# Kernel optimization log

Hardware: AMD Instinct MI355X
Metric: run time of the kernel (lower is better)

## Reference

```python
import jax, jax.numpy as jnp
import numpy as np


def setup_inputs() -> dict:
    key = jax.random.key(0)
    k1, k2, k3, k4 = jax.random.split(key, 4)
    B, H, W, C, NCLS = 128, 14, 14, 512, 200
    # post-ReLU-like non-negative feature map
    x = jax.random.uniform(k1, (B, H, W, C), dtype=jnp.float32)
    # one-hot-like logits for ground-truth labels (only argmax is used)
    gt = jax.random.normal(k2, (B, NCLS), dtype=jnp.float32)
    # positional template codebook; index [H, W] (== shape[0]-1) is the sentinel
    # 'negative' template used for all-zero channels
    t_p = jax.random.normal(k3, (H + 1, W + 1, H, W), dtype=jnp.float32)
    # per-class channel template, broadcast-multiplied with masked features
    class_templates = jax.random.uniform(k4, (NCLS, H, W, C), dtype=jnp.float32)
    return {"x": x, "gt": gt, "t_p": t_p, "class_templates": class_templates}


def reference(x, gt, t_p, class_templates):
    # x: [B, H, W, C] channels-last feature map
    B, H, W, C = x.shape
    flat = x.reshape(B, H * W, C)
    # global spatial argmax per (batch, channel) == max_pool_with_argmax over full extent
    idx = jnp.argmax(flat, axis=1)            # [B, C]
    h = idx // W                               # [B, C]
    w = idx % W                                # [B, C]
    # channels whose spatial max is exactly 0 get the sentinel template index
    empty = jnp.max(flat, axis=1) == 0.0       # [B, C]
    sentinel = t_p.shape[0] - 1
    h = jnp.where(empty, sentinel, h)
    w = jnp.where(empty, sentinel, w)
    # gather positional templates: [B, C, H, W] -> [B, H, W, C]
    templates = jnp.transpose(t_p[h, w], (0, 2, 3, 1))
    masked = jax.nn.relu(x * templates)
    # training branch with gt, reduce_loss=False: mask by the class template
    cls = jnp.argmax(gt, axis=1)               # [B]
    masked = masked * class_templates[cls]     # [B, H, W, C]
    return (masked, x, templates)
```

## Files before the change

### kernel.cpp

```cpp
#include <hip/hip_runtime.h>

#define B    128
#define H    14
#define W    14
#define C    512
#define NCLS 200
#define HW   (H * W)
#define TP_DIM 15
#define SENT_OFF ((14 * TP_DIM + 14) * HW)

typedef float  v4f __attribute__((ext_vector_type(4)));
typedef int    v4i __attribute__((ext_vector_type(4)));

__global__ __launch_bounds__(512, 4) void fused_kernel(
        const float* __restrict__ x,
        const float* __restrict__ gt,
        const float* __restrict__ t_p,
        const float* __restrict__ ctpl,
        float*       __restrict__ out) {
    __shared__ v4f s_best[14][32];
    __shared__ v4i s_idx[14][32];
    __shared__ int s_off[128];
    __shared__ int s_cls;

    const int tid     = threadIdx.x;
    const int b       = blockIdx.x >> 2;
    const int quarter = blockIdx.x & 3;
    const int cg      = tid & 31;
    const int sl      = tid >> 5;
    const int c0      = quarter * 128 + cg * 4;

    const float* __restrict__ xp = x + (size_t)b * HW * C + c0;

    if (sl < 14) {
        const int sbeg = sl * 14;
        v4f best = *(const v4f*)(xp + (size_t)sbeg * C);
        v4i bidx = (v4i){sbeg, sbeg, sbeg, sbeg};
#pragma unroll
        for (int k = 1; k < 14; ++k) {
            const int s = sbeg + k;
            v4f v = *(const v4f*)(xp + (size_t)s * C);
            if (v.x > best.x) { best.x = v.x; bidx.x = s; }
            if (v.y > best.y) { best.y = v.y; bidx.y = s; }
            if (v.z > best.z) { best.z = v.z; bidx.z = s; }
            if (v.w > best.w) { best.w = v.w; bidx.w = s; }
        }
        s_best[sl][cg] = best;
        s_idx[sl][cg]  = bidx;
    } else {
        const int lane = tid - 448;
        const float* __restrict__ g = gt + (size_t)b * NCLS;
        float gb = -__builtin_inff();
        int   gi = NCLS;
        for (int i = lane; i < NCLS; i += 64) {
            float v = g[i];
            if (v > gb) { gb = v; gi = i; }
        }
#pragma unroll
        for (int d = 1; d < 64; d <<= 1) {
            float ov = __shfl_xor(gb, d);
            int   oi = __shfl_xor(gi, d);
            if (ov > gb || (ov == gb && oi < gi)) { gb = ov; gi = oi; }
        }
        if (lane == 0) s_cls = gi;
    }
    __syncthreads();

    if (tid < 32) {
        v4f cb = s_best[0][tid];
        v4i ci = s_idx[0][tid];
#pragma unroll
        for (int k = 1; k < 14; ++k) {
            v4f p = s_best[k][tid];
            v4i q = s_idx[k][tid];
            if (p.x > cb.x) { cb.x = p.x; ci.x = q.x; }
            if (p.y > cb.y) { cb.y = p.y; ci.y = q.y; }
            if (p.z > cb.z) { cb.z = p.z; ci.z = q.z; }
            if (p.w > cb.w) { cb.w = p.w; ci.w = q.w; }
        }
        v4i o;
        o.x = (cb.x == 0.0f) ? SENT_OFF : ((ci.x / W) * TP_DIM + (ci.x % W)) * HW;
        o.y = (cb.y == 0.0f) ? SENT_OFF : ((ci.y / W) * TP_DIM + (ci.y % W)) * HW;
        o.z = (cb.z == 0.0f) ? SENT_OFF : ((ci.z / W) * TP_DIM + (ci.z % W)) * HW;
        o.w = (cb.w == 0.0f) ? SENT_OFF : ((ci.w / W) * TP_DIM + (ci.w % W)) * HW;
        *(v4i*)&s_off[tid * 4] = o;
    }
    __syncthreads();

    const int klass = s_cls;
    const v4i off   = *(const v4i*)&s_off[cg * 4];

    const size_t plane = (size_t)B * HW * C;
    const float* __restrict__ ctp = ctpl + (size_t)klass * HW * C;

    for (int q = sl; q < 49; q += 16) {
        const int s0 = q * 4;

        v4f t0 = *(const v4f*)(t_p + off.x + s0);
        v4f t1 = *(const v4f*)(t_p + off.y + s0);
        v4f t2 = *(const v4f*)(t_p + off.z + s0);
        v4f t3 = *(const v4f*)(t_p + off.w + s0);
        v4f tv[4];
        tv[0] = (v4f){t0.x, t1.x, t2.x, t3.x};
        tv[1] = (v4f){t0.y, t1.y, t2.y, t3.y};
        tv[2] = (v4f){t0.z, t1.z, t2.z, t3.z};
        tv[3] = (v4f){t0.w, t1.w, t2.w, t3.w};

        const size_t base = ((size_t)b * HW + s0) * C + c0;
        const float* __restrict__ xq = x + base;
        const float* __restrict__ cp = ctp + (size_t)s0 * C + c0;
        float* __restrict__ out_m = out + base;
        float* __restrict__ out_x = out + plane + base;
        float* __restrict__ out_t = out + 2 * plane + base;

#pragma unroll
        for (int i = 0; i < 4; ++i) {
            v4f xv = *(const v4f*)(xq + (size_t)i * C);
            v4f ct = *(const v4f*)(cp + (size_t)i * C);
            v4f tt = tv[i];
            v4f m;
            m.x = fmaxf(xv.x * tt.x, 0.0f) * ct.x;
            m.y = fmaxf(xv.y * tt.y, 0.0f) * ct.y;
            m.z = fmaxf(xv.z * tt.z, 0.0f) * ct.z;
            m.w = fmaxf(xv.w * tt.w, 0.0f) * ct.w;
            __builtin_nontemporal_store(m,  (v4f*)(out_m + (size_t)i * C));
            __builtin_nontemporal_store(xv, (v4f*)(out_x + (size_t)i * C));
            __builtin_nontemporal_store(tt, (v4f*)(out_t + (size_t)i * C));
        }
    }
}

extern "C" void kernel_launch(void* const* d_in, const int* in_sizes, int n_in,
                              void* d_out, int out_size, void* d_ws, size_t ws_size,
                              hipStream_t stream) {
    const float* x    = (const float*)d_in[0];
    const float* gt   = (const float*)d_in[1];
    const float* t_p  = (const float*)d_in[2];
    const float* ctpl = (const float*)d_in[3];
    float* out = (float*)d_out;

    hipLaunchKernelGGL(fused_kernel,
                       dim3(4 * B), dim3(512), 0, stream,
                       x, gt, t_p, ctpl, out);
}
```

Baseline: 260.4 us.

## Stage gathered templates through LDS transpose and reorder block-to-batch mapping

Replaces the per-thread scattered 4-channel template gathers and register transpose with a cooperative load of each channel's template row into a shared-memory tile. The tile is aliased with the phase-1 reduction buffers through a union and filled in two halves. Later threads read it channel-contiguous. The block index mapping changes so consecutive blocks cover different batches of the same channel quarter, and the occupancy hint is removed from the launch bounds. This adds two extra barriers and LDS traffic, possibly with bank conflicts, in exchange for more coalesced global reads of t_p.

```diff
diff --git a/kernel.cpp b/kernel.cpp
--- a/kernel.cpp
+++ b/kernel.cpp
@@ -12,23 +12,26 @@
 typedef float  v4f __attribute__((ext_vector_type(4)));
 typedef int    v4i __attribute__((ext_vector_type(4)));
 
-__global__ __launch_bounds__(512, 4) void fused_kernel(
+__global__ __launch_bounds__(512) void fused_kernel(
         const float* __restrict__ x,
         const float* __restrict__ gt,
         const float* __restrict__ t_p,
         const float* __restrict__ ctpl,
         float*       __restrict__ out) {
-    __shared__ v4f s_best[14][32];
-    __shared__ v4i s_idx[14][32];
+    __shared__ union SMem {
+        struct { v4f best[14][32]; v4i idx[14][32]; } ph1;
+        float t_tile[100][128];
+    } smem;
     __shared__ int s_off[128];
     __shared__ int s_cls;
 
     const int tid     = threadIdx.x;
-    const int b       = blockIdx.x >> 2;
-    const int quarter = blockIdx.x & 3;
+    const int b       = blockIdx.x & 127;
+    const int quarter = blockIdx.x >> 7;
     const int cg      = tid & 31;
     const int sl      = tid >> 5;
     const int c0      = quarter * 128 + cg * 4;
+    const int cl      = cg * 4;
 
     const float* __restrict__ xp = x + (size_t)b * HW * C + c0;
 
@@ -45,8 +48,8 @@
             if (v.z > best.z) { best.z = v.z; bidx.z = s; }
             if (v.w > best.w) { best.w = v.w; bidx.w = s; }
         }
-        s_best[sl][cg] = best;
-        s_idx[sl][cg]  = bidx;
+        smem.ph1.best[sl][cg] = best;
+        smem.ph1.idx[sl][cg]  = bidx;
     } else {
         const int lane = tid - 448;
         const float* __restrict__ g = gt + (size_t)b * NCLS;
@@ -67,12 +70,12 @@
     __syncthreads();
 
     if (tid < 32) {
-        v4f cb = s_best[0][tid];
-        v4i ci = s_idx[0][tid];
+        v4f cb = smem.ph1.best[0][tid];
+        v4i ci = smem.ph1.idx[0][tid];
 #pragma unroll
         for (int k = 1; k < 14; ++k) {
-            v4f p = s_best[k][tid];
-            v4i q = s_idx[k][tid];
+            v4f p = smem.ph1.best[k][tid];
+            v4i q = smem.ph1.idx[k][tid];
             if (p.x > cb.x) { cb.x = p.x; ci.x = q.x; }
             if (p.y > cb.y) { cb.y = p.y; ci.y = q.y; }
             if (p.z > cb.z) { cb.z = p.z; ci.z = q.z; }
@@ -88,23 +91,30 @@
     __syncthreads();
 
     const int klass = s_cls;
-    const v4i off   = *(const v4i*)&s_off[cg * 4];
-
     const size_t plane = (size_t)B * HW * C;
     const float* __restrict__ ctp = ctpl + (size_t)klass * HW * C;
 
-    for (int q = sl; q < 49; q += 16) {
+    const int r = tid >> 2;
+    const int p = tid & 3;
+    const float* __restrict__ trow = t_p + s_off[r];
+
+    auto stage = [&](int jbeg, int jend, int sbase) {
+        for (int j = jbeg + p; j < jend; j += 4) {
+            v4f v = *(const v4f*)(trow + j * 4);
+            const int s = j * 4 - sbase;
+            smem.t_tile[s + 0][r] = v.x;
+            smem.t_tile[s + 1][r] = v.y;
+            smem.t_tile[s + 2][r] = v.z;
+            smem.t_tile[s + 3][r] = v.w;
+        }
+    };
+
+    auto process_quad = [&](int q, int sbase) {
         const int s0 = q * 4;
-
-        v4f t0 = *(const v4f*)(t_p + off.x + s0);
-        v4f t1 = *(const v4f*)(t_p + off.y + s0);
-        v4f t2 = *(const v4f*)(t_p + off.z + s0);
-        v4f t3 = *(const v4f*)(t_p + off.w + s0);
-        v4f tv[4];
-        tv[0] = (v4f){t0.x, t1.x, t2.x, t3.x};
-        tv[1] = (v4f){t0.y, t1.y, t2.y, t3.y};
-        tv[2] = (v4f){t0.z, t1.z, t2.z, t3.z};
-        tv[3] = (v4f){t0.w, t1.w, t2.w, t3.w};
+        v4f tvv[4];
+#pragma unroll
+        for (int i = 0; i < 4; ++i)
+            tvv[i] = *(const v4f*)&smem.t_tile[s0 - sbase + i][cl];
 
         const size_t base = ((size_t)b * HW + s0) * C + c0;
         const float* __restrict__ xq = x + base;
@@ -117,7 +127,7 @@
         for (int i = 0; i < 4; ++i) {
             v4f xv = *(const v4f*)(xq + (size_t)i * C);
             v4f ct = *(const v4f*)(cp + (size_t)i * C);
-            v4f tt = tv[i];
+            v4f tt = tvv[i];
             v4f m;
             m.x = fmaxf(xv.x * tt.x, 0.0f) * ct.x;
             m.y = fmaxf(xv.y * tt.y, 0.0f) * ct.y;
@@ -127,7 +137,18 @@
             __builtin_nontemporal_store(xv, (v4f*)(out_x + (size_t)i * C));
             __builtin_nontemporal_store(tt, (v4f*)(out_t + (size_t)i * C));
         }
-    }
+    };
+
+    stage(0, 24, 0);
+    __syncthreads();
+    process_quad(sl, 0);
+    if (sl < 8) process_quad(sl + 16, 0);
+    __syncthreads();
+
+    stage(24, 49, 96);
+    __syncthreads();
+    process_quad(24 + sl, 96);
+    if (sl <= 8) process_quad(40 + sl, 96);
 }
 
 extern "C" void kernel_launch(void* const* d_in, const int* in_sizes, int n_in,
```

Result: faster. 250.3 us (-3.9%).

## Keep x tile in registers across argmax and output phases, swizzle block order

Applied to the files above, without the earlier changes.

Each warp-row now loads its 12 (or 16) spatial rows of x into registers once, uses them for the per-thread argmax, and reuses them for the masked-output and x-copy writes instead of reading x again from global memory. All 16 warp-rows take part in the argmax, and the gt argmax moves to a separate wave after the first barrier. Block indexing changes so consecutive blocks cover different batches of the same channel quarter, and the occupancy hint in launch_bounds is dropped. The cost is many more live registers (the xr array), which may lower occupancy.

```diff
diff --git a/kernel.cpp b/kernel.cpp
--- a/kernel.cpp
+++ b/kernel.cpp
@@ -12,43 +12,85 @@
 typedef float  v4f __attribute__((ext_vector_type(4)));
 typedef int    v4i __attribute__((ext_vector_type(4)));
 
-__global__ __launch_bounds__(512, 4) void fused_kernel(
+__global__ __launch_bounds__(512) void fused_kernel(
         const float* __restrict__ x,
         const float* __restrict__ gt,
         const float* __restrict__ t_p,
         const float* __restrict__ ctpl,
         float*       __restrict__ out) {
-    __shared__ v4f s_best[14][32];
-    __shared__ v4i s_idx[14][32];
+    __shared__ v4f s_best[16][32];
+    __shared__ v4i s_idx[16][32];
     __shared__ int s_off[128];
     __shared__ int s_cls;
 
     const int tid     = threadIdx.x;
-    const int b       = blockIdx.x >> 2;
-    const int quarter = blockIdx.x & 3;
+    const int b       = blockIdx.x & 127;
+    const int quarter = blockIdx.x >> 7;
     const int cg      = tid & 31;
     const int sl      = tid >> 5;
     const int c0      = quarter * 128 + cg * 4;
+    const int cl      = cg * 4;
+    const bool extra  = (sl == 15);
+    const int  sbeg   = 12 * sl;
 
     const float* __restrict__ xp = x + (size_t)b * HW * C + c0;
 
-    if (sl < 14) {
-        const int sbeg = sl * 14;
-        v4f best = *(const v4f*)(xp + (size_t)sbeg * C);
-        v4i bidx = (v4i){sbeg, sbeg, sbeg, sbeg};
+    v4f xr[16];
 #pragma unroll
-        for (int k = 1; k < 14; ++k) {
+    for (int k = 0; k < 12; ++k)
+        xr[k] = *(const v4f*)(xp + (size_t)(sbeg + k) * C);
+    if (extra) {
+#pragma unroll
+        for (int k = 12; k < 16; ++k)
+            xr[k] = *(const v4f*)(xp + (size_t)(sbeg + k) * C);
+    }
+
+    v4f best = xr[0];
+    v4i bidx = (v4i){sbeg, sbeg, sbeg, sbeg};
+#pragma unroll
+    for (int k = 1; k < 12; ++k) {
+        const int s = sbeg + k;
+        v4f v = xr[k];
+        if (v.x > best.x) { best.x = v.x; bidx.x = s; }
+        if (v.y > best.y) { best.y = v.y; bidx.y = s; }
+        if (v.z > best.z) { best.z = v.z; bidx.z = s; }
+        if (v.w > best.w) { best.w = v.w; bidx.w = s; }
+    }
+    if (extra) {
+#pragma unroll
+        for (int k = 12; k < 16; ++k) {
             const int s = sbeg + k;
-            v4f v = *(const v4f*)(xp + (size_t)s * C);
+            v4f v = xr[k];
             if (v.x > best.x) { best.x = v.x; bidx.x = s; }
             if (v.y > best.y) { best.y = v.y; bidx.y = s; }
             if (v.z > best.z) { best.z = v.z; bidx.z = s; }
             if (v.w > best.w) { best.w = v.w; bidx.w = s; }
         }
-        s_best[sl][cg] = best;
-        s_idx[sl][cg]  = bidx;
-    } else {
-        const int lane = tid - 448;
+    }
+    s_best[sl][cg] = best;
+    s_idx[sl][cg]  = bidx;
+    __syncthreads();
+
+    if (tid < 32) {
+        v4f cb = s_best[0][tid];
+        v4i ci = s_idx[0][tid];
+#pragma unroll
+        for (int k = 1; k < 16; ++k) {
+            v4f p = s_best[k][tid];
+            v4i q = s_idx[k][tid];
+            if (p.x > cb.x) { cb.x = p.x; ci.x = q.x; }
+            if (p.y > cb.y) { cb.y = p.y; ci.y = q.y; }
+            if (p.z > cb.z) { cb.z = p.z; ci.z = q.z; }
+            if (p.w > cb.w) { cb.w = p.w; ci.w = q.w; }
+        }
+        v4i o;
+        o.x = (cb.x == 0.0f) ? SENT_OFF : ((ci.x / W) * TP_DIM + (ci.x % W)) * HW;
+        o.y = (cb.y == 0.0f) ? SENT_OFF : ((ci.y / W) * TP_DIM + (ci.y % W)) * HW;
+        o.z = (cb.z == 0.0f) ? SENT_OFF : ((ci.z / W) * TP_DIM + (ci.z % W)) * HW;
+        o.w = (cb.w == 0.0f) ? SENT_OFF : ((ci.w / W) * TP_DIM + (ci.w % W)) * HW;
+        *(v4i*)&s_off[tid * 4] = o;
+    } else if (tid >= 64 && tid < 128) {
+        const int lane = tid - 64;
         const float* __restrict__ g = gt + (size_t)b * NCLS;
         float gb = -__builtin_inff();
         int   gi = NCLS;
@@ -66,48 +108,32 @@
     }
     __syncthreads();
 
-    if (tid < 32) {
-        v4f cb = s_best[0][tid];
-        v4i ci = s_idx[0][tid];
+    const int klass = s_cls;
+    const v4i off = *(const v4i*)&s_off[cl];
+
+    v4f tr[4][4];
 #pragma unroll
-        for (int k = 1; k < 14; ++k) {
-            v4f p = s_best[k][tid];
-            v4i q = s_idx[k][tid];
-            if (p.x > cb.x) { cb.x = p.x; ci.x = q.x; }
-            if (p.y > cb.y) { cb.y = p.y; ci.y = q.y; }
-            if (p.z > cb.z) { cb.z = p.z; ci.z = q.z; }
-            if (p.w > cb.w) { cb.w = p.w; ci.w = q.w; }
-        }
-        v4i o;
-        o.x = (cb.x == 0.0f) ? SENT_OFF : ((ci.x / W) * TP_DIM + (ci.x % W)) * HW;
-        o.y = (cb.y == 0.0f) ? SENT_OFF : ((ci.y / W) * TP_DIM + (ci.y % W)) * HW;
-        o.z = (cb.z == 0.0f) ? SENT_OFF : ((ci.z / W) * TP_DIM + (ci.z % W)) * HW;
-        o.w = (cb.w == 0.0f) ? SENT_OFF : ((ci.w / W) * TP_DIM + (ci.w % W)) * HW;
-        *(v4i*)&s_off[tid * 4] = o;
+    for (int m = 0; m < 3; ++m) {
+        tr[0][m] = *(const v4f*)(t_p + off.x + sbeg + 4 * m);
+        tr[1][m] = *(const v4f*)(t_p + off.y + sbeg + 4 * m);
+        tr[2][m] = *(const v4f*)(t_p + off.z + sbeg + 4 * m);
+        tr[3][m] = *(const v4f*)(t_p + off.w + sbeg + 4 * m);
     }
-    __syncthreads();
-
-    const int klass = s_cls;
-    const v4i off   = *(const v4i*)&s_off[cg * 4];
+    if (extra) {
+        tr[0][3] = *(const v4f*)(t_p + off.x + sbeg + 12);
+        tr[1][3] = *(const v4f*)(t_p + off.y + sbeg + 12);
+        tr[2][3] = *(const v4f*)(t_p + off.z + sbeg + 12);
+        tr[3][3] = *(const v4f*)(t_p + off.w + sbeg + 12);
+    }
 
     const size_t plane = (size_t)B * HW * C;
     const float* __restrict__ ctp = ctpl + (size_t)klass * HW * C;
 
-    for (int q = sl; q < 49; q += 16) {
-        const int s0 = q * 4;
-
-        v4f t0 = *(const v4f*)(t_p + off.x + s0);
-        v4f t1 = *(const v4f*)(t_p + off.y + s0);
-        v4f t2 = *(const v4f*)(t_p + off.z + s0);
-        v4f t3 = *(const v4f*)(t_p + off.w + s0);
-        v4f tv[4];
-        tv[0] = (v4f){t0.x, t1.x, t2.x, t3.x};
-        tv[1] = (v4f){t0.y, t1.y, t2.y, t3.y};
-        tv[2] = (v4f){t0.z, t1.z, t2.z, t3.z};
-        tv[3] = (v4f){t0.w, t1.w, t2.w, t3.w};
-
+#pragma unroll
+    for (int m = 0; m < 4; ++m) {
+        if (m == 3 && !extra) break;
+        const int s0 = sbeg + 4 * m;
         const size_t base = ((size_t)b * HW + s0) * C + c0;
-        const float* __restrict__ xq = x + base;
         const float* __restrict__ cp = ctp + (size_t)s0 * C + c0;
         float* __restrict__ out_m = out + base;
         float* __restrict__ out_x = out + plane + base;
@@ -115,15 +141,19 @@
 
 #pragma unroll
         for (int i = 0; i < 4; ++i) {
-            v4f xv = *(const v4f*)(xq + (size_t)i * C);
+            v4f xv = xr[4 * m + i];
             v4f ct = *(const v4f*)(cp + (size_t)i * C);
-            v4f tt = tv[i];
-            v4f m;
-            m.x = fmaxf(xv.x * tt.x, 0.0f) * ct.x;
-            m.y = fmaxf(xv.y * tt.y, 0.0f) * ct.y;
-            m.z = fmaxf(xv.z * tt.z, 0.0f) * ct.z;
-            m.w = fmaxf(xv.w * tt.w, 0.0f) * ct.w;
-            __builtin_nontemporal_store(m,  (v4f*)(out_m + (size_t)i * C));
+            v4f tt;
+            tt.x = tr[0][m][i];
+            tt.y = tr[1][m][i];
+            tt.z = tr[2][m][i];
+            tt.w = tr[3][m][i];
+            v4f mm;
+            mm.x = fmaxf(xv.x * tt.x, 0.0f) * ct.x;
+            mm.y = fmaxf(xv.y * tt.y, 0.0f) * ct.y;
+            mm.z = fmaxf(xv.z * tt.z, 0.0f) * ct.z;
+            mm.w = fmaxf(xv.w * tt.w, 0.0f) * ct.w;
+            __builtin_nontemporal_store(mm, (v4f*)(out_m + (size_t)i * C));
             __builtin_nontemporal_store(xv, (v4f*)(out_x + (size_t)i * C));
             __builtin_nontemporal_store(tt, (v4f*)(out_t + (size_t)i * C));
         }
```

Result: no change. 256.9 us (-1.3%).
